# Kernel optimization log

Hardware: AMD Instinct MI355X
Metric: run time of the kernel (lower is better)

## Reference

```python
import jax, jax.numpy as jnp
import numpy as np

N = 50000      # num_labels (nodes)
HID = 64       # hidden_dim
HEADS = 4
CH = 16        # hidden_dim // 4 per head
R = 4          # relations
E = 200000     # edges per relation
DEPTH = 2
SLOPE = 0.2    # GATv2 leaky_relu negative slope
EPS = 1e-5     # LayerNorm eps


def layer_norm(x, g, b):
    mu = jnp.mean(x, axis=-1, keepdims=True)
    var = jnp.mean((x - mu) ** 2, axis=-1, keepdims=True)
    return (x - mu) / jnp.sqrt(var + EPS) * g + b


def setup_inputs() -> dict:
    key = jax.random.key(0)
    ks = jax.random.split(key, 8)
    # edges with src != dst (PyG remove_self_loops is then a no-op)
    src = jax.random.randint(ks[0], (R, E), 0, N, dtype=jnp.int32)
    off = jax.random.randint(ks[1], (R, E), 1, N, dtype=jnp.int32)
    dst = ((src + off) % N).astype(jnp.int32)
    edge_index = jnp.stack([src, dst], axis=1)  # [R, 2, E]
    s = 1.0 / np.sqrt(HID)
    return {
        "label_embeddings": jax.random.normal(ks[2], (N, HID), jnp.float32) * 0.5,
        "entry_w": jax.random.normal(ks[3], (HID, HID), jnp.float32) * s,
        "entry_b": jnp.zeros((HID,), jnp.float32),
        "entry_ln_g": jnp.ones((HID,), jnp.float32),
        "entry_ln_b": jnp.zeros((HID,), jnp.float32),
        "conv_wl": jax.random.normal(ks[4], (DEPTH, R, HID, HEADS * CH), jnp.float32) * s,
        "conv_wr": jax.random.normal(ks[5], (DEPTH, R, HID, HEADS * CH), jnp.float32) * s,
        "conv_att": jax.random.normal(ks[6], (DEPTH, R, HEADS, CH), jnp.float32) * (1.0 / np.sqrt(CH)),
        "conv_bias": jnp.zeros((DEPTH, R, HEADS * CH), jnp.float32),
        "norm_g": jnp.ones((HID,), jnp.float32),
        "norm_b": jnp.zeros((HID,), jnp.float32),
        "edge_index": edge_index,
    }


def _gatv2_layer(x, wl, wr, att, bias, src, dst):
    """One GATv2Conv over one relation. x:[N,HID]; returns [N, HEADS*CH]."""
    xl = (x @ wl).reshape(N, HEADS, CH)  # source transform
    xr = (x @ wr).reshape(N, HEADS, CH)  # target transform
    m = xl[src] + xr[dst]                          # [E+N, HEADS, CH]
    e = jnp.einsum('ehc,hc->eh', jax.nn.leaky_relu(m, SLOPE), att)  # [E+N, HEADS]
    # segment softmax over incoming edges of each dst node
    emax = jax.ops.segment_max(e, dst, num_segments=N)  # [N, HEADS]
    a = jnp.exp(e - emax[dst])
    denom = jax.ops.segment_sum(a, dst, num_segments=N)
    alpha = a / denom[dst]                          # every node has a self-loop -> denom > 0
    msg = xl[src] * alpha[..., None]                # [E+N, HEADS, CH]
    out = jax.ops.segment_sum(msg, dst, num_segments=N).reshape(N, HEADS * CH)
    return out + bias


def reference(label_embeddings, entry_w, entry_b, entry_ln_g, entry_ln_b,
              conv_wl, conv_wr, conv_att, conv_bias, norm_g, norm_b, edge_index):
    x = jax.nn.gelu(layer_norm(label_embeddings @ entry_w + entry_b, entry_ln_g, entry_ln_b),
                    approximate=False)
    loop = jnp.arange(N, dtype=edge_index.dtype)
    for layer in range(DEPTH):
        outs = []
        for r in range(R):
            src = jnp.concatenate([edge_index[r, 0], loop])  # add self-loops (PyG default)
            dst = jnp.concatenate([edge_index[r, 1], loop])
            outs.append(_gatv2_layer(x, conv_wl[layer, r], conv_wr[layer, r],
                                     conv_att[layer, r], conv_bias[layer, r], src, dst))
        x = sum(outs) / R                              # HeteroConv aggr='mean'
        x = layer_norm(jax.nn.gelu(x, approximate=False), norm_g, norm_b)  # dropout = identity (eval)
    return x
```

## Files before the change

### kernel.cpp

```cpp
#include <hip/hip_runtime.h>
#include <hip/hip_bf16.h>

#define NN 50000
#define RR 4
#define EE 200000

typedef __hip_bfloat16 bf16;
typedef __attribute__((ext_vector_type(8))) short short8;
typedef __attribute__((ext_vector_type(4))) float float4v;
typedef __attribute__((ext_vector_type(2))) float float2v;

__device__ __forceinline__ unsigned short f2bu(float v) {
    bf16 h = __float2bfloat16(v);
    return *(unsigned short*)&h;
}
__device__ __forceinline__ float ldf(const void* p, int i, int isbf) {
    return isbf ? __bfloat162float(((const bf16*)p)[i]) : ((const float*)p)[i];
}
__device__ __forceinline__ int dtype_isbf(const void* lg) {
    return ((const unsigned*)lg)[0] == 0x3F803F80u;
}
__device__ __forceinline__ float gelu_exact(float x) {
    return 0.5f * x * (1.0f + erff(x * 0.70710678118654752f));
}
__device__ __forceinline__ float2v bp2(unsigned u) {
    float2v f;
    f.x = __uint_as_float(u << 16);
    f.y = __uint_as_float(u & 0xffff0000u);
    return f;
}
__device__ __forceinline__ float2v lrelu2(float2v m) {
    float2v s = m * 0.2f;
    float2v r;
    r.x = fmaxf(m.x, s.x);
    r.y = fmaxf(m.y, s.y);
    return r;
}

#define PW_ENTRY_W 0
#define PW_ENTRY_B 4096
#define PW_LN_G    4160
#define PW_LN_B    4224
#define PW_WL      4288
#define PW_ATT     69824
#define PW_BIAS    70336
#define PW_NG      70848
#define PW_NB      70912
#define PW_TOT     70976

#define WT_ELEMS (2 * RR * 128 * 64)
#define SCAN_N (RR * NN)
#define NSB 196
#define SCANA_PB 49

#define HIST_BLOCKS 782
#define CVT_BLOCKS  196
#define ENTRY_BLOCKS 2500
#define ENTRY_WAVES (ENTRY_BLOCKS * 4)
__global__ __launch_bounds__(256) void mega1_k(const int* __restrict__ ei,
                                               int* __restrict__ cnt,
                                               unsigned char* __restrict__ slot8,
                                               const void* __restrict__ emb,
                                               const void* ew, const void* eb,
                                               const void* lg, const void* lb,
                                               const void* wl, const void* wr,
                                               const void* at, const void* bi,
                                               const void* ng, const void* nb,
                                               float* __restrict__ P,
                                               bf16* __restrict__ WT,
                                               bf16* __restrict__ xout) {
    int b = blockIdx.x;
    int t = threadIdx.x;
    int isbf = dtype_isbf(lg);
    if (b < HIST_BLOCKS) {
        int base = b * 1024 + t;
#pragma unroll
        for (int j = 0; j < 4; j++) {
            int idx = base + j * 256;
            if (idx < RR * EE) {
                int r = idx / EE;
                int e = idx - r * EE;
                int d = ei[r * 2 * EE + EE + e];
                int p = atomicAdd(&cnt[r * NN + d], 1);
                slot8[idx] = (unsigned char)p;
            }
        }
        return;
    }
    if (b < HIST_BLOCKS + CVT_BLOCKS) {
#pragma unroll
        for (int j = 0; j < 4; j++) {
            int i = (b - HIST_BLOCKS) * 1024 + j * 256 + t;
            if (i < WT_ELEMS) {
                int k = i & 63;
                int c = (i >> 6) & 127;
                int lr = i >> 13;
                float v = (c < 64) ? ldf(wl, (lr * 64 + k) * 64 + c, isbf)
                                   : ldf(wr, (lr * 64 + k) * 64 + (c - 64), isbf);
                WT[i] = __float2bfloat16(v);
            }
            if (i < PW_TOT) {
                const void* src = nullptr;
                int off = 0;
                if (i < PW_ENTRY_B)      { src = ew; off = i - PW_ENTRY_W; }
                else if (i < PW_LN_G)    { src = eb; off = i - PW_ENTRY_B; }
                else if (i < PW_LN_B)    { src = lg; off = i - PW_LN_G; }
                else if (i < PW_WL)      { src = lb; off = i - PW_LN_B; }
                else if (i < PW_ATT)     { src = nullptr; }
                else if (i < PW_BIAS)    { src = at; off = i - PW_ATT; }
                else if (i < PW_NG)      { src = bi; off = i - PW_BIAS; }
                else if (i < PW_NB)      { src = ng; off = i - PW_NG; }
                else                     { src = nb; off = i - PW_NB; }
                if (src) P[i] = ldf(src, off, isbf);
            }
        }
        return;
    }
    int wv = (b - HIST_BLOCKS - CVT_BLOCKS) * 4 + (t >> 6);
    int c = t & 63;
    for (int j = 0; j < 5; j++) {
        int node = wv + j * ENTRY_WAVES;
        float ev = ldf(emb, node * 64 + c, isbf);
        float acc = 0.f;
#pragma unroll 8
        for (int k = 0; k < 64; k++) {
            float xv = __shfl(ev, k, 64);
            acc += xv * ldf(ew, k * 64 + c, isbf);
        }
        acc += ldf(eb, c, isbf);
        float s = acc;
#pragma unroll
        for (int m = 1; m < 64; m <<= 1) s += __shfl_xor(s, m, 64);
        float mu = s * (1.f / 64.f);
        float d = acc - mu;
        float vs = d * d;
#pragma unroll
        for (int m = 1; m < 64; m <<= 1) vs += __shfl_xor(vs, m, 64);
        float var = vs * (1.f / 64.f);
        float y = d * rsqrtf(var + 1e-5f) * ldf(lg, c, isbf) + ldf(lb, c, isbf);
        xout[node * 64 + c] = __float2bfloat16(gelu_exact(y));
    }
}

__global__ void scanB_k(int* __restrict__ bsum, int* __restrict__ rp) {
    int l = threadIdx.x;
    int i0 = l * 4;
    int v0 = (i0 + 0 < NSB) ? bsum[i0 + 0] : 0;
    int v1 = (i0 + 1 < NSB) ? bsum[i0 + 1] : 0;
    int v2 = (i0 + 2 < NSB) ? bsum[i0 + 2] : 0;
    int v3 = (i0 + 3 < NSB) ? bsum[i0 + 3] : 0;
    int ts = v0 + v1 + v2 + v3;
    int inc = ts;
#pragma unroll
    for (int m = 1; m < 64; m <<= 1) {
        int y = __shfl_up(inc, m, 64);
        if (l >= m) inc += y;
    }
    int run = inc - ts;
    if (i0 + 0 < NSB) { bsum[i0 + 0] = run; run += v0; }
    if (i0 + 1 < NSB) { bsum[i0 + 1] = run; run += v1; }
    if (i0 + 2 < NSB) { bsum[i0 + 2] = run; run += v2; }
    if (i0 + 3 < NSB) { bsum[i0 + 3] = run; run += v3; }
    if (l == 63) rp[SCAN_N] = inc;
}

__global__ __launch_bounds__(256) void scanC_k(const int* __restrict__ cnt,
                                               const int* __restrict__ bsum,
                                               int* __restrict__ rp) {
    int b = blockIdx.x, t = threadIdx.x;
    int i0 = b * 1024 + t * 4;
    int v0 = (i0 + 0 < SCAN_N) ? cnt[i0 + 0] : 0;
    int v1 = (i0 + 1 < SCAN_N) ? cnt[i0 + 1] : 0;
    int v2 = (i0 + 2 < SCAN_N) ? cnt[i0 + 2] : 0;
    int v3 = (i0 + 3 < SCAN_N) ? cnt[i0 + 3] : 0;
    int ts = v0 + v1 + v2 + v3;
    int lane = t & 63, w = t >> 6;
    int inc = ts;
#pragma unroll
    for (int m = 1; m < 64; m <<= 1) {
        int y = __shfl_up(inc, m, 64);
        if (lane >= m) inc += y;
    }
    __shared__ int ws[4];
    if (lane == 63) ws[w] = inc;
    __syncthreads();
    int run = bsum[b];
    for (int k = 0; k < w; k++) run += ws[k];
    run += inc - ts;
    if (i0 + 0 < SCAN_N) { rp[i0 + 0] = run; run += v0; }
    if (i0 + 1 < SCAN_N) { rp[i0 + 1] = run; run += v1; }
    if (i0 + 2 < SCAN_N) { rp[i0 + 2] = run; run += v2; }
    if (i0 + 3 < SCAN_N) { rp[i0 + 3] = run; run += v3; }
}

__global__ __launch_bounds__(256) void scat_k(const int* __restrict__ ei,
                                              const unsigned char* __restrict__ slot8,
                                              const int* __restrict__ rp,
                                              unsigned short* __restrict__ col) {
    int bx = blockIdx.x, r = blockIdx.y;
    const int* eis = ei + r * 2 * EE;
#pragma unroll
    for (int j = 0; j < 4; j++) {
        int e = bx * 1024 + j * 256 + threadIdx.x;
        if (e < EE) {
            int s = eis[e];
            int d = eis[EE + e];
            int p = slot8[r * EE + e];
            col[rp[r * NN + d] + p] = (unsigned short)s;
        }
    }
}

#define GR 80
__global__ __launch_bounds__(256) void gemm_m(const bf16* __restrict__ X,
                                              const bf16* __restrict__ WTlayer,
                                              bf16* __restrict__ xlB,
                                              bf16* __restrict__ xrB,
                                              const int* __restrict__ cnt,
                                              int* __restrict__ bsum,
                                              int scanBlk) {
    int bx = blockIdx.x;
    int r = blockIdx.y;
    __shared__ float sh[16 * 132];
    if (bx < scanBlk) {
        int a = r * scanBlk + bx;
        int t = threadIdx.x;
        int s = 0;
#pragma unroll
        for (int j = 0; j < 4; j++) {
            int i = a * 1024 + j * 256 + t;
            if (i < SCAN_N) s += cnt[i];
        }
#pragma unroll
        for (int m = 1; m < 64; m <<= 1) s += __shfl_xor(s, m, 64);
        if ((t & 63) == 0) sh[t >> 6] = __int_as_float(s);
        __syncthreads();
        if (t == 0)
            bsum[a] = __float_as_int(sh[0]) + __float_as_int(sh[1]) +
                      __float_as_int(sh[2]) + __float_as_int(sh[3]);
        return;
    }
    const short* Xs = (const short*)X;
    const short* WT = (const short*)(WTlayer + (size_t)r * 8192);
    bf16* xl = xlB + (size_t)r * NN * 64;
    bf16* xr = xrB + (size_t)r * NN * 64;

    int t = threadIdx.x;
    int w = t >> 6;
    int lane = t & 63;
    int m = lane & 15, kq = lane >> 4;
    int row0 = (bx - scanBlk) * GR;

    short8 b0[2], b1[2];
    int c0t[2];
#pragma unroll
    for (int tile = 0; tile < 2; tile++) {
        int ct = w * 2 + tile;
        int c0 = ct * 16 + m;
        c0t[tile] = c0;
        const short* bp = WT + c0 * 64 + kq * 8;
        b0[tile] = *(const short8*)bp;
        b1[tile] = *(const short8*)(bp + 32);
    }

    const short* ap = Xs + (row0 + m) * 64 + kq * 8;
    short8 a0 = *(const short8*)ap;
    short8 a1 = *(const short8*)(ap + 32);

    for (int g = 0; g < 5; g++) {
        short8 na0, na1;
        if (g < 4) {
            const short* np = ap + (g + 1) * 16 * 64;
            na0 = *(const short8*)np;
            na1 = *(const short8*)(np + 32);
        }
#pragma unroll
        for (int tile = 0; tile < 2; tile++) {
            float4v acc = {0.f, 0.f, 0.f, 0.f};
            asm volatile(
                "v_mfma_f32_16x16x32_bf16 %0, %1, %2, %0\n\t"
                "v_mfma_f32_16x16x32_bf16 %0, %3, %4, %0\n\t"
                "s_nop 7\n\t"
                "s_nop 7"
                : "+v"(acc)
                : "v"(a0), "v"(b0[tile]), "v"(a1), "v"(b1[tile]));
#pragma unroll
            for (int i = 0; i < 4; i++) sh[(kq * 4 + i) * 132 + c0t[tile]] = acc[i];
        }
        __syncthreads();
        {
            int row = t >> 4, cg = (t & 15) * 8;
            float v0 = sh[row * 132 + cg + 0], v1 = sh[row * 132 + cg + 1];
            float v2 = sh[row * 132 + cg + 2], v3 = sh[row * 132 + cg + 3];
            float v4 = sh[row * 132 + cg + 4], v5 = sh[row * 132 + cg + 5];
            float v6 = sh[row * 132 + cg + 6], v7 = sh[row * 132 + cg + 7];
            uint4 u;
            u.x = ((unsigned)f2bu(v1) << 16) | f2bu(v0);
            u.y = ((unsigned)f2bu(v3) << 16) | f2bu(v2);
            u.z = ((unsigned)f2bu(v5) << 16) | f2bu(v4);
            u.w = ((unsigned)f2bu(v7) << 16) | f2bu(v6);
            size_t grow = row0 + g * 16 + row;
            if (cg < 64) *(uint4*)&xl[grow * 64 + cg] = u;
            else         *(uint4*)&xr[grow * 64 + (cg - 64)] = u;
        }
        __syncthreads();
        a0 = na0; a1 = na1;
    }
}

__device__ __forceinline__ void edge_accum(uint4 u0, uint4 u1, bool act,
                                           const float2v at2[8], const float2v xr2[8],
                                           float2v A2[8], float& D) {
    float2v x2[8];
    x2[0] = bp2(u0.x); x2[1] = bp2(u0.y); x2[2] = bp2(u0.z); x2[3] = bp2(u0.w);
    x2[4] = bp2(u1.x); x2[5] = bp2(u1.y); x2[6] = bp2(u1.z); x2[7] = bp2(u1.w);
    float2v t2 = (float2v){0.f, 0.f};
#pragma unroll
    for (int i = 0; i < 8; i++)
        t2 = t2 + lrelu2(x2[i] + xr2[i]) * at2[i];
    float tt = t2.x + t2.y;
    float p = act ? exp2f(tt) : 0.f;
    D += p;
    float2v p2 = (float2v){p, p};
#pragma unroll
    for (int i = 0; i < 8; i++) A2[i] = A2[i] + p2 * x2[i];
}

__global__ __launch_bounds__(256) void aggfin_k(const bf16* __restrict__ xlB,
                                                const bf16* __restrict__ xrB,
                                                const float* __restrict__ attL,
                                                const float* __restrict__ biasL,
                                                const int* __restrict__ rp,
                                                const unsigned short* __restrict__ col,
                                                const float* __restrict__ P,
                                                const void* __restrict__ lg,
                                                void* __restrict__ outp,
                                                int finalOut) {
    __shared__ float shRes[RR][4][68];
    int t = threadIdx.x;
    int r = t >> 6;
    int lane = t & 63;
    int nodeBase = blockIdx.x * 4;
    int nn = lane >> 4, es = (lane >> 2) & 3, h = lane & 3;
    int node = nodeBase + nn;

    const unsigned* xl = (const unsigned*)(xlB + (size_t)r * NN * 64);
    const unsigned* xr = (const unsigned*)(xrB + (size_t)r * NN * 64);
    const float* att = attL + r * 64;
    const float* bias = biasL + r * 64;

    int idx = r * NN + node;
    int base = rp[idx];
    int cn = rp[idx + 1] - base;
    const uint4* qr = (const uint4*)(xr + (size_t)node * 32 + h * 8);
    uint4 r0 = qr[0], r1 = qr[1];

    const unsigned short* bucket = col + base;
    int c0raw = (es > 0) ? (int)bucket[es - 1] : node;
    int c1raw = (int)bucket[es + 3];

    unsigned s0 = (unsigned)c0raw < (unsigned)NN ? (unsigned)c0raw : (unsigned)(NN - 1);
    unsigned s1 = (unsigned)c1raw < (unsigned)NN ? (unsigned)c1raw : (unsigned)(NN - 1);
    const uint4* q0 = (const uint4*)(xl + (size_t)s0 * 32 + h * 8);
    uint4 u0 = q0[0], u1 = q0[1];
    const uint4* q1 = (const uint4*)(xl + (size_t)s1 * 32 + h * 8);
    uint4 w0 = q1[0], w1 = q1[1];

    float2v at2[8], xr2[8];
    {
        const float4* apv = (const float4*)(att + h * 16);
#pragma unroll
        for (int i = 0; i < 4; i++) {
            float4 a = apv[i];
            at2[2 * i].x = a.x * 1.44269504f; at2[2 * i].y = a.y * 1.44269504f;
            at2[2 * i + 1].x = a.z * 1.44269504f; at2[2 * i + 1].y = a.w * 1.44269504f;
        }
        xr2[0] = bp2(r0.x); xr2[1] = bp2(r0.y); xr2[2] = bp2(r0.z); xr2[3] = bp2(r0.w);
        xr2[4] = bp2(r1.x); xr2[5] = bp2(r1.y); xr2[6] = bp2(r1.z); xr2[7] = bp2(r1.w);
    }
    int total = cn + 1;
    int kmax = total;
    kmax = max(kmax, __shfl_xor(kmax, 16, 64));
    kmax = max(kmax, __shfl_xor(kmax, 32, 64));

    float2v A2[8];
#pragma unroll
    for (int i = 0; i < 8; i++) A2[i] = (float2v){0.f, 0.f};
    float D = 0.f;

    edge_accum(u0, u1, es < total, at2, xr2, A2, D);
    edge_accum(w0, w1, es + 4 < total, at2, xr2, A2, D);

    for (int k = es + 8; k < kmax; k += 4) {
        bool act = k < total;
        int sr = act ? (int)bucket[k - 1] : node;
        const uint4* q = (const uint4*)(xl + (size_t)sr * 32 + h * 8);
        uint4 t0 = q[0], t1 = q[1];
        edge_accum(t0, t1, act, at2, xr2, A2, D);
    }

    D += __shfl_xor(D, 4, 64);
    D += __shfl_xor(D, 8, 64);
#pragma unroll
    for (int i = 0; i < 8; i++) {
        A2[i].x += __shfl_xor(A2[i].x, 4, 64);
        A2[i].x += __shfl_xor(A2[i].x, 8, 64);
        A2[i].y += __shfl_xor(A2[i].y, 4, 64);
        A2[i].y += __shfl_xor(A2[i].y, 8, 64);
    }
    if (es == 0) {
        float inv = __builtin_amdgcn_rcpf(D);
        const float4* bp = (const float4*)(bias + h * 16);
        float* dst = &shRes[r][nn][h * 16];
#pragma unroll
        for (int i = 0; i < 4; i++) {
            float4 b = bp[i];
            dst[4 * i + 0] = A2[2 * i].x * inv + b.x;
            dst[4 * i + 1] = A2[2 * i].y * inv + b.y;
            dst[4 * i + 2] = A2[2 * i + 1].x * inv + b.z;
            dst[4 * i + 3] = A2[2 * i + 1].y * inv + b.w;
        }
    }
    __syncthreads();
    int wn = t >> 6, c = t & 63;
    float v = shRes[0][wn][c] + shRes[1][wn][c] + shRes[2][wn][c] + shRes[3][wn][c];
    v = gelu_exact(v * 0.25f);
    float s = v;
#pragma unroll
    for (int m = 1; m < 64; m <<= 1) s += __shfl_xor(s, m, 64);
    float mu = s * (1.f / 64.f);
    float d = v - mu;
    float vs = d * d;
#pragma unroll
    for (int m = 1; m < 64; m <<= 1) vs += __shfl_xor(vs, m, 64);
    float var = vs * (1.f / 64.f);
    float y = d * rsqrtf(var + 1e-5f) * P[PW_NG + c] + P[PW_NB + c];
    size_t o = (size_t)(nodeBase + wn) * 64 + c;
    if (!finalOut) {
        ((bf16*)outp)[o] = __float2bfloat16(y);
    } else {
        if (dtype_isbf(lg)) ((bf16*)outp)[o] = __float2bfloat16(y);
        else                ((float*)outp)[o] = y;
    }
}

extern "C" void kernel_launch(void* const* d_in, const int* in_sizes, int n_in,
                              void* d_out, int out_size, void* d_ws, size_t ws_size,
                              hipStream_t stream) {
    const void* emb = d_in[0];
    const void* lg  = d_in[3];
    const int*  ei  = (const int*)d_in[11];

    const size_t BUF = (size_t)NN * 64;

    bf16* X   = (bf16*)d_ws;
    bf16* XL  = X + BUF;
    bf16* XR  = XL + RR * BUF;
    bf16* WT  = XR + RR * BUF;
    float* P  = (float*)(WT + WT_ELEMS);
    int* cnt  = (int*)(P + PW_TOT);
    int* rp   = cnt + SCAN_N;
    int* bsum = rp + SCAN_N + 1;
    unsigned short* col = (unsigned short*)(bsum + 256);
    unsigned char* slot8 = (unsigned char*)(col + RR * EE + 64);

    hipMemsetAsync(cnt, 0, SCAN_N * sizeof(int), stream);

    mega1_k<<<HIST_BLOCKS + CVT_BLOCKS + ENTRY_BLOCKS, 256, 0, stream>>>(
        ei, cnt, slot8, emb, d_in[1], d_in[2], d_in[3], d_in[4], d_in[5], d_in[6],
        d_in[7], d_in[8], d_in[9], d_in[10], P, WT, X);

    int nodeBlocks = NN / 4;

    gemm_m<<<dim3(SCANA_PB + 625, RR), 256, 0, stream>>>(
        X, WT, XL, XR, cnt, bsum, SCANA_PB);
    scanB_k<<<1, 64, 0, stream>>>(bsum, rp);
    scanC_k<<<NSB, 256, 0, stream>>>(cnt, bsum, rp);
    scat_k<<<dim3(196, RR), 256, 0, stream>>>(ei, slot8, rp, col);

    aggfin_k<<<nodeBlocks, 256, 0, stream>>>(
        XL, XR, P + PW_ATT, P + PW_BIAS, rp, col, P, lg, (void*)X, 0);

    gemm_m<<<dim3(625, RR), 256, 0, stream>>>(
        X, WT + (size_t)RR * 8192, XL, XR, cnt, bsum, 0);
    aggfin_k<<<nodeBlocks, 256, 0, stream>>>(
        XL, XR, P + PW_ATT + RR * 64, P + PW_BIAS + RR * 64, rp, col, P, lg, d_out, 1);
}
```

Measured before the change: 335.1 us.

## Use LDS range-partitioned histogram and fuse edge scatter into first GEMM launch

The degree histogram moves from global atomics to per-block shared-memory counters, with each block covering one relation and a 6250-node destination range. This removes the memset and the contended global atomics, but every block now reads the full dst array of its relation. The block-sum scan becomes a separate kernel, and the col scatter is folded into the first GEMM launch so it runs alongside the layer-0 transform. The mega kernel moves to 1024-thread blocks, so the histogram work runs on only 32 blocks, which risks low parallelism for that phase.

```diff
diff --git a/kernel.cpp b/kernel.cpp
--- a/kernel.cpp
+++ b/kernel.cpp
@@ -51,13 +51,13 @@
 #define WT_ELEMS (2 * RR * 128 * 64)
 #define SCAN_N (RR * NN)
 #define NSB 196
-#define SCANA_PB 49
-
-#define HIST_BLOCKS 782
-#define CVT_BLOCKS  196
-#define ENTRY_BLOCKS 2500
-#define ENTRY_WAVES (ENTRY_BLOCKS * 4)
-__global__ __launch_bounds__(256) void mega1_k(const int* __restrict__ ei,
+
+#define HIST_BLOCKS 32
+#define RANGE_N 6250
+#define CVT_BLOCKS 18
+#define ENTRY_BLOCKS 625
+#define ENTRY_WAVES 10000
+__global__ __launch_bounds__(1024) void mega_k(const int* __restrict__ ei,
                                                int* __restrict__ cnt,
                                                unsigned char* __restrict__ slot8,
                                                const void* __restrict__ emb,
@@ -73,24 +73,31 @@
     int t = threadIdx.x;
     int isbf = dtype_isbf(lg);
     if (b < HIST_BLOCKS) {
-        int base = b * 1024 + t;
+        __shared__ unsigned hc[RANGE_N];
+        int r = b >> 3, rg = b & 7;
+        for (int i = t; i < RANGE_N; i += 1024) hc[i] = 0u;
+        __syncthreads();
+        const uint4* dst4 = (const uint4*)(ei + r * 2 * EE + EE);
+        unsigned base = rg * RANGE_N;
+        unsigned char* sl = slot8 + (size_t)r * EE;
+        for (int q = t; q < EE / 4; q += 1024) {
+            uint4 d4 = dst4[q];
+            int e = q * 4;
+            unsigned x;
+            x = d4.x - base; if (x < RANGE_N) sl[e + 0] = (unsigned char)atomicAdd(&hc[x], 1u);
+            x = d4.y - base; if (x < RANGE_N) sl[e + 1] = (unsigned char)atomicAdd(&hc[x], 1u);
+            x = d4.z - base; if (x < RANGE_N) sl[e + 2] = (unsigned char)atomicAdd(&hc[x], 1u);
+            x = d4.w - base; if (x < RANGE_N) sl[e + 3] = (unsigned char)atomicAdd(&hc[x], 1u);
+        }
+        __syncthreads();
+        int* cp = cnt + r * NN + base;
+        for (int i = t; i < RANGE_N; i += 1024) cp[i] = (int)hc[i];
+        return;
+    }
+    if (b < HIST_BLOCKS + CVT_BLOCKS) {
 #pragma unroll
         for (int j = 0; j < 4; j++) {
-            int idx = base + j * 256;
-            if (idx < RR * EE) {
-                int r = idx / EE;
-                int e = idx - r * EE;
-                int d = ei[r * 2 * EE + EE + e];
-                int p = atomicAdd(&cnt[r * NN + d], 1);
-                slot8[idx] = (unsigned char)p;
-            }
-        }
-        return;
-    }
-    if (b < HIST_BLOCKS + CVT_BLOCKS) {
-#pragma unroll
-        for (int j = 0; j < 4; j++) {
-            int i = (b - HIST_BLOCKS) * 1024 + j * 256 + t;
+            int i = (b - HIST_BLOCKS) * 4096 + j * 1024 + t;
             if (i < WT_ELEMS) {
                 int k = i & 63;
                 int c = (i >> 6) & 127;
@@ -116,7 +123,7 @@
         }
         return;
     }
-    int wv = (b - HIST_BLOCKS - CVT_BLOCKS) * 4 + (t >> 6);
+    int wv = (b - HIST_BLOCKS - CVT_BLOCKS) * 16 + (t >> 6);
     int c = t & 63;
     for (int j = 0; j < 5; j++) {
         int node = wv + j * ENTRY_WAVES;
@@ -140,6 +147,23 @@
         float y = d * rsqrtf(var + 1e-5f) * ldf(lg, c, isbf) + ldf(lb, c, isbf);
         xout[node * 64 + c] = __float2bfloat16(gelu_exact(y));
     }
+}
+
+__global__ __launch_bounds__(256) void scanA_k(const int* __restrict__ cnt,
+                                               int* __restrict__ bsum) {
+    int b = blockIdx.x, t = threadIdx.x;
+    int s = 0;
+#pragma unroll
+    for (int j = 0; j < 4; j++) {
+        int i = b * 1024 + j * 256 + t;
+        if (i < SCAN_N) s += cnt[i];
+    }
+#pragma unroll
+    for (int m = 1; m < 64; m <<= 1) s += __shfl_xor(s, m, 64);
+    __shared__ int ws[4];
+    if ((t & 63) == 0) ws[t >> 6] = s;
+    __syncthreads();
+    if (t == 0) bsum[b] = ws[0] + ws[1] + ws[2] + ws[3];
 }
 
 __global__ void scanB_k(int* __restrict__ bsum, int* __restrict__ rp) {
@@ -193,51 +217,30 @@
     if (i0 + 3 < SCAN_N) { rp[i0 + 3] = run; run += v3; }
 }
 
-__global__ __launch_bounds__(256) void scat_k(const int* __restrict__ ei,
-                                              const unsigned char* __restrict__ slot8,
-                                              const int* __restrict__ rp,
-                                              unsigned short* __restrict__ col) {
-    int bx = blockIdx.x, r = blockIdx.y;
-    const int* eis = ei + r * 2 * EE;
-#pragma unroll
-    for (int j = 0; j < 4; j++) {
-        int e = bx * 1024 + j * 256 + threadIdx.x;
-        if (e < EE) {
-            int s = eis[e];
-            int d = eis[EE + e];
-            int p = slot8[r * EE + e];
-            col[rp[r * NN + d] + p] = (unsigned short)s;
-        }
-    }
-}
-
 #define GR 80
 __global__ __launch_bounds__(256) void gemm_m(const bf16* __restrict__ X,
                                               const bf16* __restrict__ WTlayer,
                                               bf16* __restrict__ xlB,
                                               bf16* __restrict__ xrB,
-                                              const int* __restrict__ cnt,
-                                              int* __restrict__ bsum,
-                                              int scanBlk) {
+                                              const int* __restrict__ ei,
+                                              const unsigned char* __restrict__ slot8,
+                                              const int* __restrict__ rp,
+                                              unsigned short* __restrict__ col,
+                                              int scatBlk) {
     int bx = blockIdx.x;
     int r = blockIdx.y;
-    __shared__ float sh[16 * 132];
-    if (bx < scanBlk) {
-        int a = r * scanBlk + bx;
-        int t = threadIdx.x;
-        int s = 0;
+    if (bx < scatBlk) {
+        const int* eis = ei + r * 2 * EE;
 #pragma unroll
         for (int j = 0; j < 4; j++) {
-            int i = a * 1024 + j * 256 + t;
-            if (i < SCAN_N) s += cnt[i];
-        }
-#pragma unroll
-        for (int m = 1; m < 64; m <<= 1) s += __shfl_xor(s, m, 64);
-        if ((t & 63) == 0) sh[t >> 6] = __int_as_float(s);
-        __syncthreads();
-        if (t == 0)
-            bsum[a] = __float_as_int(sh[0]) + __float_as_int(sh[1]) +
-                      __float_as_int(sh[2]) + __float_as_int(sh[3]);
+            int e = bx * 1024 + j * 256 + threadIdx.x;
+            if (e < EE) {
+                int s = eis[e];
+                int d = eis[EE + e];
+                int p = slot8[(size_t)r * EE + e];
+                col[rp[r * NN + d] + p] = (unsigned short)s;
+            }
+        }
         return;
     }
     const short* Xs = (const short*)X;
@@ -245,11 +248,12 @@
     bf16* xl = xlB + (size_t)r * NN * 64;
     bf16* xr = xrB + (size_t)r * NN * 64;
 
+    __shared__ float sh[16 * 132];
     int t = threadIdx.x;
     int w = t >> 6;
     int lane = t & 63;
     int m = lane & 15, kq = lane >> 4;
-    int row0 = (bx - scanBlk) * GR;
+    int row0 = (bx - scatBlk) * GR;
 
     short8 b0[2], b1[2];
     int c0t[2];
@@ -464,25 +468,23 @@
     unsigned short* col = (unsigned short*)(bsum + 256);
     unsigned char* slot8 = (unsigned char*)(col + RR * EE + 64);
 
-    hipMemsetAsync(cnt, 0, SCAN_N * sizeof(int), stream);
-
-    mega1_k<<<HIST_BLOCKS + CVT_BLOCKS + ENTRY_BLOCKS, 256, 0, stream>>>(
+    mega_k<<<HIST_BLOCKS + CVT_BLOCKS + ENTRY_BLOCKS, 1024, 0, stream>>>(
         ei, cnt, slot8, emb, d_in[1], d_in[2], d_in[3], d_in[4], d_in[5], d_in[6],
         d_in[7], d_in[8], d_in[9], d_in[10], P, WT, X);
 
-    int nodeBlocks = NN / 4;
-
-    gemm_m<<<dim3(SCANA_PB + 625, RR), 256, 0, stream>>>(
-        X, WT, XL, XR, cnt, bsum, SCANA_PB);
+    scanA_k<<<NSB, 256, 0, stream>>>(cnt, bsum);
     scanB_k<<<1, 64, 0, stream>>>(bsum, rp);
     scanC_k<<<NSB, 256, 0, stream>>>(cnt, bsum, rp);
-    scat_k<<<dim3(196, RR), 256, 0, stream>>>(ei, slot8, rp, col);
-
+
+    int nodeBlocks = NN / 4;
+
+    gemm_m<<<dim3(196 + 625, RR), 256, 0, stream>>>(
+        X, WT, XL, XR, ei, slot8, rp, col, 196);
     aggfin_k<<<nodeBlocks, 256, 0, stream>>>(
         XL, XR, P + PW_ATT, P + PW_BIAS, rp, col, P, lg, (void*)X, 0);
 
     gemm_m<<<dim3(625, RR), 256, 0, stream>>>(
-        X, WT + (size_t)RR * 8192, XL, XR, cnt, bsum, 0);
+        X, WT + (size_t)RR * 8192, XL, XR, ei, slot8, rp, col, 0);
     aggfin_k<<<nodeBlocks, 256, 0, stream>>>(
         XL, XR, P + PW_ATT + RR * 64, P + PW_BIAS + RR * 64, rp, col, P, lg, d_out, 1);
 }
```

Result: faster. 306.7 us (-8.5%).
